# Performance work log

Measured on AMD Instinct MI355X. Metric: run time of the kernel, lower is better.

## Reference

```python
import jax, jax.numpy as jnp
import numpy as np

BN_EPS = 1e-5
W_SCALE = 0.05  # keep pre-softmax logits in a sane range with random weights


def setup_inputs() -> dict:
    key = jax.random.key(0)
    ks = jax.random.split(key, 8)
    b, C, H, W = 2, 512, 80, 80
    Ck, Cv, Co = 256, 256, 512
    return {
        "x": jax.random.normal(ks[0], (b, C, H, W), dtype=jnp.float32),
        "wk": jax.random.normal(ks[1], (Ck, C), dtype=jnp.float32) * W_SCALE,
        "bk": jax.random.normal(ks[2], (Ck,), dtype=jnp.float32) * W_SCALE,
        "gamma": jnp.ones((Ck,), dtype=jnp.float32),
        "beta": jnp.zeros((Ck,), dtype=jnp.float32),
        "rmean": jnp.zeros((Ck,), dtype=jnp.float32),
        "rvar": jnp.ones((Ck,), dtype=jnp.float32),
        "wv": jax.random.normal(ks[3], (Cv, C), dtype=jnp.float32) * W_SCALE,
        "bv": jax.random.normal(ks[4], (Cv,), dtype=jnp.float32) * W_SCALE,
        "wW": jax.random.normal(ks[5], (Co, Cv), dtype=jnp.float32) * W_SCALE,
        "bW": jax.random.normal(ks[6], (Co,), dtype=jnp.float32) * W_SCALE,
    }


def reference(x, wk, bk, gamma, beta, rmean, rvar, wv, bv, wW, bW):
    b, C, H, Wd = x.shape
    N = H * Wd
    Ck = wk.shape[0]
    Cv = wv.shape[0]
    # f_key == f_query (shared module): 1x1 conv + BN(inference) + ReLU
    k = jnp.einsum('bchw,oc->bohw', x, wk) + bk[:, None, None]
    scale_bn = gamma / jnp.sqrt(rvar + BN_EPS)
    k = (k - rmean[:, None, None]) * scale_bn[:, None, None] + beta[:, None, None]
    k = jax.nn.relu(k).reshape(b, Ck, N)          # [b, Ck, N]
    q = jnp.transpose(k, (0, 2, 1))               # [b, N, Ck] (query shares weights with key)
    # f_value: plain 1x1 conv
    v = (jnp.einsum('bchw,oc->bohw', x, wv) + bv[:, None, None]).reshape(b, Cv, N)
    sim = jnp.einsum('bnc,bcm->bnm', q, k) * (Ck ** -0.5)  # [b, N, N]
    sim = jax.nn.softmax(sim, axis=-1)
    ctx = jnp.einsum('bnm,bvm->bvn', sim, v).reshape(b, Cv, H, Wd)
    out = jnp.einsum('bvhw,ov->bohw', ctx, wW) + bW[:, None, None]
    return out
```

## Files before the change

kernel.cpp:

```cpp
#include <hip/hip_runtime.h>
#include <stdint.h>

typedef __attribute__((ext_vector_type(8))) short bf16x8;
typedef __attribute__((ext_vector_type(4))) float f32x4;

__device__ __forceinline__ ushort f2bf(float f) {
    union { float f; uint32_t i; } v; v.f = f;
    uint32_t r = v.i + 0x7fff + ((v.i >> 16) & 1);
    return (ushort)(r >> 16);
}
__device__ __forceinline__ uint32_t cvtpk(float lo, float hi) {
    uint32_t r;
    asm("v_cvt_pk_bf16_f32 %0, %1, %2" : "=v"(r) : "v"(lo), "v"(hi));
    return r;
}

typedef unsigned int uint_as1 __attribute__((address_space(1)));
typedef unsigned int uint_as3 __attribute__((address_space(3)));
__device__ __forceinline__ void async16(const void* g, void* l) {
    __builtin_amdgcn_global_load_lds((const uint_as1*)g, (uint_as3*)l, 16, 0, 0);
}


__global__ void cvt_f32_bf16(const float* __restrict__ in, ushort* __restrict__ out, int n) {
    int i = blockIdx.x * blockDim.x + threadIdx.x;
    if (i < n) out[i] = f2bf(in[i]);
}

__global__ void prep_bn(const float* __restrict__ bk, const float* __restrict__ gamma,
                        const float* __restrict__ beta, const float* __restrict__ rmean,
                        const float* __restrict__ rvar,
                        float* __restrict__ scaleA, float* __restrict__ shiftA) {
    int i = threadIdx.x;
    float s = gamma[i] * rsqrtf(rvar[i] + 1e-5f);
    scaleA[i] = 0.25f * s;
    shiftA[i] = 0.25f * ((bk[i] - rmean[i]) * s + beta[i]);
}

__global__ void transpose_cvt(const float* __restrict__ x, ushort* __restrict__ xt) {
    __shared__ float t[32][33];
    int b = blockIdx.z;
    int n0 = blockIdx.x * 32, c0 = blockIdx.y * 32;
    const float* xb = x + (size_t)b * 512 * 6400;
    ushort* xtb = xt + (size_t)b * 6400 * 512;
    int tx = threadIdx.x, ty = threadIdx.y;
    t[ty][tx] = xb[(size_t)(c0 + ty) * 6400 + n0 + tx];
    __syncthreads();
    xtb[(size_t)(n0 + ty) * 512 + c0 + tx] = f2bf(t[tx][ty]);
}

template <int EPI>
__global__ __launch_bounds__(256) void gemm_nt(
    const ushort* __restrict__ A, const ushort* __restrict__ B, void* __restrict__ Cout,
    int K, int lda, int ldb, int ldc,
    size_t zsa, size_t zsb, size_t zsc,
    const float* __restrict__ vec0, const float* __restrict__ vec1,
    float* __restrict__ rsum) {
    __shared__ __align__(16) ushort smem[6 * 4096];

    A += (size_t)blockIdx.z * zsa;
    B += (size_t)blockIdx.z * zsb;

    const int tid = threadIdx.x;
    const int lane = tid & 63, wave = tid >> 6;
    const int wm = wave & 1, wn = wave >> 1;
    const int bM = blockIdx.y * 128, bN = blockIdx.x * 128;

    const int sr = lane >> 2;
    const int scs = ((lane & 3) ^ ((lane >> 3) & 3)) * 8;
    const ushort* gA0 = A + (size_t)(bM + wave * 32 + sr) * lda + scs;
    const ushort* gA1 = gA0 + (size_t)16 * lda;
    const ushort* gB0 = B + (size_t)(bN + wave * 32 + sr) * ldb + scs;
    const ushort* gB1 = gB0 + (size_t)16 * ldb;
    ushort* lAw = &smem[wave * 1024];
    ushort* lBw = &smem[3 * 4096 + wave * 1024];

    const int rowA = wm * 64;
    const int rowB = wn * 64;
    const int fr = lane & 15;
    const int fk = ((lane >> 4) ^ ((fr >> 1) & 3)) * 8;

    f32x4 acc[4][4] = {};
    const int nT = K >> 5;

    auto stage = [&](int t, int buf) {
        const int k0 = t * 32;
        const int ob = buf * 4096;
        async16(gA0 + k0, lAw + ob);
        async16(gA1 + k0, lAw + ob + 512);
        async16(gB0 + k0, lBw + ob);
        async16(gB1 + k0, lBw + ob + 512);
    };

    stage(0, 0);
    if (nT > 1) stage(1, 1);

    for (int t = 0; t < nT; ++t) {
        if (t + 1 < nT) { asm volatile("s_waitcnt vmcnt(4)" ::: "memory"); }
        else            { asm volatile("s_waitcnt vmcnt(0)" ::: "memory"); }
        __builtin_amdgcn_sched_barrier(0);
        __builtin_amdgcn_s_barrier();
        __builtin_amdgcn_sched_barrier(0);
        if (t + 2 < nT) stage(t + 2, (t + 2) % 3);
        const int cur = t % 3;
        const ushort* lA = &smem[cur * 4096];
        const ushort* lB = &smem[3 * 4096 + cur * 4096];
        bf16x8 af[4], bff[4];
#pragma unroll
        for (int mi = 0; mi < 4; mi++)
            af[mi] = *(const bf16x8*)&lA[(rowA + mi * 16 + fr) * 32 + fk];
#pragma unroll
        for (int ni = 0; ni < 4; ni++)
            bff[ni] = *(const bf16x8*)&lB[(rowB + ni * 16 + fr) * 32 + fk];
#pragma unroll
        for (int mi = 0; mi < 4; mi++)
#pragma unroll
            for (int ni = 0; ni < 4; ni++)
                acc[mi][ni] = __builtin_amdgcn_mfma_f32_16x16x32_bf16(af[mi], bff[ni], acc[mi][ni], 0, 0, 0);
        __builtin_amdgcn_sched_barrier(0);
    }
    __builtin_amdgcn_s_barrier();
    __builtin_amdgcn_sched_barrier(0);

    float* Cf = (float*)Cout + (size_t)blockIdx.z * zsc;
    ushort* Cu = (ushort*)Cout + (size_t)blockIdx.z * zsc;
    float* lt = (float*)smem;
    const int g4 = (lane >> 4) * 4;
    const int cl = lane & 15;
    const int lr = tid >> 3;
    const int ch = tid & 7;

#pragma unroll
    for (int mi = 0; mi < 4; ++mi) {
#pragma unroll
        for (int ni = 0; ni < 4; ++ni) {
            const int lcol = wn * 64 + ni * 16 + cl;
#pragma unroll
            for (int r = 0; r < 4; ++r)
                lt[(wm * 16 + g4 + r) * 132 + lcol] = acc[mi][ni][r];
        }
        __syncthreads();
        {
            const int brow = (lr < 16) ? (mi * 16 + lr) : (64 + mi * 16 + (lr - 16));
            const int grow = bM + brow;
            const int gcol = bN + ch * 16;
            float vv[16];
#pragma unroll
            for (int i = 0; i < 16; i += 4) {
                f32x4 q = *(const f32x4*)&lt[lr * 132 + ch * 16 + i];
                vv[i] = q[0]; vv[i + 1] = q[1]; vv[i + 2] = q[2]; vv[i + 3] = q[3];
            }
            if (EPI == 1) {
#pragma unroll
                for (int i = 0; i < 16; i++)
                    vv[i] = fmaxf(vv[i] * vec0[gcol + i] + vec1[gcol + i], 0.f);
            }
            if (EPI == 2 || EPI == 3) {
                const float rb = vec0[grow];
#pragma unroll
                for (int i = 0; i < 16; i++) vv[i] += rb;
            }
            if (EPI == 5) {
                float ssum = 0.f;
#pragma unroll
                for (int i = 0; i < 16; i++) { vv[i] = __expf(vv[i]); ssum += vv[i]; }
                ssum += __shfl_down(ssum, 4, 8);
                ssum += __shfl_down(ssum, 2, 8);
                ssum += __shfl_down(ssum, 1, 8);
                if (ch == 0) rsum[(size_t)blockIdx.x * 6400 + grow] = ssum;
            }
            if (EPI == 3 || EPI == 4) {
#pragma unroll
                for (int i = 0; i < 16; i += 4) {
                    f32x4 q = { vv[i], vv[i + 1], vv[i + 2], vv[i + 3] };
                    *(f32x4*)&Cf[(size_t)grow * ldc + gcol + i] = q;
                }
            } else {
                uint4 q0 = { cvtpk(vv[0], vv[1]), cvtpk(vv[2], vv[3]),
                             cvtpk(vv[4], vv[5]), cvtpk(vv[6], vv[7]) };
                uint4 q1 = { cvtpk(vv[8], vv[9]), cvtpk(vv[10], vv[11]),
                             cvtpk(vv[12], vv[13]), cvtpk(vv[14], vv[15]) };
                *(uint4*)&Cu[(size_t)grow * ldc + gcol] = q0;
                *(uint4*)&Cu[(size_t)grow * ldc + gcol + 8] = q1;
            }
        }
        __syncthreads();
    }
}

__global__ __launch_bounds__(256) void combine_inv(const float* __restrict__ rsum,
                                                   float* __restrict__ inv) {
    int r = blockIdx.x * 256 + threadIdx.x;
    float s = 0.f;
#pragma unroll
    for (int xb = 0; xb < 50; xb++) s += rsum[(size_t)xb * 6400 + r];
    inv[r] = 1.f / s;
}

__global__ __launch_bounds__(256) void reduce_ctx(const float* __restrict__ part, ushort* __restrict__ ctx,
                                                  const float* __restrict__ inv) {
    const size_t CH = 1638400;
    size_t i = ((size_t)blockIdx.x * 256 + threadIdx.x) * 4;
    float4 a = *(const float4*)&part[i];
#pragma unroll
    for (int c = 1; c < 5; c++) {
        float4 s = *(const float4*)&part[i + (size_t)c * CH];
        a.x += s.x; a.y += s.y; a.z += s.z; a.w += s.w;
    }
    const float w = inv[i >> 8];
    uint2 o = { cvtpk(a.x * w, a.y * w), cvtpk(a.z * w, a.w * w) };
    *(uint2*)&ctx[i] = o;
}

extern "C" void kernel_launch(void* const* d_in, const int* in_sizes, int n_in,
                              void* d_out, int out_size, void* d_ws, size_t ws_size,
                              hipStream_t stream) {
    (void)in_sizes; (void)n_in; (void)out_size; (void)ws_size;
    const float* x     = (const float*)d_in[0];
    const float* wk    = (const float*)d_in[1];
    const float* bk    = (const float*)d_in[2];
    const float* gamma = (const float*)d_in[3];
    const float* beta  = (const float*)d_in[4];
    const float* rmean = (const float*)d_in[5];
    const float* rvar  = (const float*)d_in[6];
    const float* wv    = (const float*)d_in[7];
    const float* bv    = (const float*)d_in[8];
    const float* wW    = (const float*)d_in[9];
    const float* bW    = (const float*)d_in[10];
    float* out = (float*)d_out;

    ushort* Xt   = (ushort*)d_ws;
    ushort* wkb  = Xt + 6553600;
    ushort* wvb  = wkb + 131072;
    ushort* wWb  = wvb + 131072;
    ushort* Kt   = wWb + 131072;
    ushort* V    = Kt + 3276800;
    ushort* ctxT = V + 3276800;
    ushort* S    = ctxT + 3276800;
    float* scaleA = (float*)(S + 40960000);
    float* shiftA = scaleA + 256;
    float* rowsum = shiftA + 256;
    float* inv    = rowsum + 320000;
    float* part   = inv + 6400;

    cvt_f32_bf16<<<512, 256, 0, stream>>>(wk, wkb, 131072);
    cvt_f32_bf16<<<512, 256, 0, stream>>>(wv, wvb, 131072);
    cvt_f32_bf16<<<512, 256, 0, stream>>>(wW, wWb, 131072);
    prep_bn<<<1, 256, 0, stream>>>(bk, gamma, beta, rmean, rvar, scaleA, shiftA);
    transpose_cvt<<<dim3(200, 16, 2), dim3(32, 32), 0, stream>>>(x, Xt);

    gemm_nt<1><<<dim3(2, 50, 2), 256, 0, stream>>>(Xt, wkb, Kt, 512, 512, 512, 256,
                                                   3276800, 0, 1638400, scaleA, shiftA, nullptr);
    gemm_nt<2><<<dim3(50, 2, 2), 256, 0, stream>>>(wvb, Xt, V, 512, 512, 512, 6400,
                                                   0, 3276800, 1638400, bv, nullptr, nullptr);

    for (int b = 0; b < 2; b++) {
        ushort* Ktb  = Kt + (size_t)b * 1638400;
        ushort* Vb   = V  + (size_t)b * 1638400;
        ushort* ctxb = ctxT + (size_t)b * 1638400;
        gemm_nt<5><<<dim3(50, 50), 256, 0, stream>>>(Ktb, Ktb, S, 256, 256, 256, 6400,
                                                     0, 0, 0, nullptr, nullptr, rowsum);
        combine_inv<<<25, 256, 0, stream>>>(rowsum, inv);
        gemm_nt<4><<<dim3(2, 50, 5), 256, 0, stream>>>(S, Vb, part, 1280, 6400, 6400, 256,
                                                       1280, 1280, 1638400, nullptr, nullptr, nullptr);
        reduce_ctx<<<1600, 256, 0, stream>>>(part, ctxb, inv);
    }

    gemm_nt<3><<<dim3(50, 4, 2), 256, 0, stream>>>(wWb, ctxT, out, 256, 256, 256, 6400,
                                                   0, 1638400, 3276800, bW, nullptr, nullptr);
}
```

Before: 309.5 us.

## Add dedicated P·V GEMM kernel with register-held A operand and triple-buffered B

Replaces the generic gemm_nt<4> for the softmax-probabilities × V product with a specialized kernel. A fragments (S rows) are loaded straight from global memory into registers and prefetched two steps ahead, while only B (V) tiles go to LDS through async global_load_lds into a three-stage ring with one barrier per K step. The output is staged through LDS wave by wave for coalesced fp32 stores. The aim is to cut LDS traffic and barrier stalls in the largest GEMM, at the cost of more register pressure and uncoalesced direct global reads of A.

Result: slower. 319.7 us (+3.3%).

```diff
diff --git a/kernel.cpp b/kernel.cpp
--- a/kernel.cpp
+++ b/kernel.cpp
@@ -169,7 +169,7 @@
                 ssum += __shfl_down(ssum, 1, 8);
                 if (ch == 0) rsum[(size_t)blockIdx.x * 6400 + grow] = ssum;
             }
-            if (EPI == 3 || EPI == 4) {
+            if (EPI == 3) {
 #pragma unroll
                 for (int i = 0; i < 16; i += 4) {
                     f32x4 q = { vv[i], vv[i + 1], vv[i + 2], vv[i + 3] };
@@ -185,6 +185,106 @@
             }
         }
         __syncthreads();
+    }
+}
+
+__global__ __launch_bounds__(256) void gemm_pv(
+    const ushort* __restrict__ A, const ushort* __restrict__ B, float* __restrict__ Cout,
+    int K, int lda, int ldb, int ldc,
+    size_t zsa, size_t zsb, size_t zsc) {
+    __shared__ __align__(16) ushort smem[3 * 4096];
+
+    A += (size_t)blockIdx.z * zsa;
+    B += (size_t)blockIdx.z * zsb;
+
+    const int tid = threadIdx.x;
+    const int lane = tid & 63, wave = tid >> 6;
+    const int bM = blockIdx.y * 128, bN = blockIdx.x * 128;
+
+    const int sr = lane >> 2;
+    const int scs = ((lane & 3) ^ ((lane >> 3) & 3)) * 8;
+    const ushort* gB0 = B + (size_t)(bN + wave * 32 + sr) * ldb + scs;
+    const ushort* gB1 = gB0 + (size_t)16 * ldb;
+    ushort* lBw = &smem[wave * 1024];
+
+    const int fr = lane & 15;
+    const int fq = lane >> 4;
+    const int fk = (fq ^ ((fr >> 1) & 3)) * 8;
+
+    const ushort* gA0 = A + (size_t)(bM + wave * 32 + fr) * lda + fq * 8;
+    const ushort* gA1 = gA0 + (size_t)16 * lda;
+
+    f32x4 acc[2][8] = {};
+    const int nT = K >> 5;
+
+    auto stageB = [&](int t, int buf) {
+        const int k0 = t * 32;
+        const int ob = buf * 4096;
+        async16(gB0 + k0, lBw + ob);
+        async16(gB1 + k0, lBw + ob + 512);
+    };
+
+    stageB(0, 0);
+    bf16x8 a0E = *(const bf16x8*)&gA0[0];
+    bf16x8 a1E = *(const bf16x8*)&gA1[0];
+    stageB(1, 1);
+    bf16x8 a0O = *(const bf16x8*)&gA0[32];
+    bf16x8 a1O = *(const bf16x8*)&gA1[32];
+
+    auto body = [&](int t, bf16x8& a0S, bf16x8& a1S) {
+        if (t + 1 < nT) { asm volatile("s_waitcnt vmcnt(4)" ::: "memory"); }
+        else            { asm volatile("s_waitcnt vmcnt(0)" ::: "memory"); }
+        __builtin_amdgcn_sched_barrier(0);
+        __builtin_amdgcn_s_barrier();
+        __builtin_amdgcn_sched_barrier(0);
+        bf16x8 u0 = a0S, u1 = a1S;
+        if (t + 2 < nT) {
+            stageB(t + 2, (t + 2) % 3);
+            const int k0 = (t + 2) * 32;
+            a0S = *(const bf16x8*)&gA0[k0];
+            a1S = *(const bf16x8*)&gA1[k0];
+        }
+        const ushort* lB = &smem[(t % 3) * 4096];
+        bf16x8 bff[8];
+#pragma unroll
+        for (int ni = 0; ni < 8; ni++)
+            bff[ni] = *(const bf16x8*)&lB[(ni * 16 + fr) * 32 + fk];
+#pragma unroll
+        for (int ni = 0; ni < 8; ni++)
+            acc[0][ni] = __builtin_amdgcn_mfma_f32_16x16x32_bf16(u0, bff[ni], acc[0][ni], 0, 0, 0);
+#pragma unroll
+        for (int ni = 0; ni < 8; ni++)
+            acc[1][ni] = __builtin_amdgcn_mfma_f32_16x16x32_bf16(u1, bff[ni], acc[1][ni], 0, 0, 0);
+        __builtin_amdgcn_sched_barrier(0);
+    };
+
+    for (int i = 0; i < nT; i += 2) {
+        body(i, a0E, a1E);
+        body(i + 1, a0O, a1O);
+    }
+
+    float* Cf = Cout + (size_t)blockIdx.z * zsc;
+    float* lt = (float*)smem;
+    const int lr = tid >> 3;
+    const int ch = tid & 7;
+#pragma unroll
+    for (int ph = 0; ph < 4; ++ph) {
+        __syncthreads();
+        if (wave == ph) {
+#pragma unroll
+            for (int mi = 0; mi < 2; ++mi)
+#pragma unroll
+                for (int ni = 0; ni < 8; ++ni)
+#pragma unroll
+                    for (int r = 0; r < 4; ++r)
+                        lt[(mi * 16 + fq * 4 + r) * 132 + ni * 16 + fr] = acc[mi][ni][r];
+        }
+        __syncthreads();
+        const int grow = bM + ph * 32 + lr;
+        const int gcol = bN + ch * 16;
+#pragma unroll
+        for (int i = 0; i < 16; i += 4)
+            *(f32x4*)&Cf[(size_t)grow * ldc + gcol + i] = *(const f32x4*)&lt[lr * 132 + ch * 16 + i];
     }
 }
 
@@ -261,8 +361,8 @@
         gemm_nt<5><<<dim3(50, 50), 256, 0, stream>>>(Ktb, Ktb, S, 256, 256, 256, 6400,
                                                      0, 0, 0, nullptr, nullptr, rowsum);
         combine_inv<<<25, 256, 0, stream>>>(rowsum, inv);
-        gemm_nt<4><<<dim3(2, 50, 5), 256, 0, stream>>>(S, Vb, part, 1280, 6400, 6400, 256,
-                                                       1280, 1280, 1638400, nullptr, nullptr, nullptr);
+        gemm_pv<<<dim3(2, 50, 5), 256, 0, stream>>>(S, Vb, part, 1280, 6400, 6400, 256,
+                                                    1280, 1280, 1638400);
         reduce_ctx<<<1600, 256, 0, stream>>>(part, ctxb, inv);
     }
 
```

## Exploit symmetry of K^T K similarity to compute only upper-triangle tiles

Applied to the files above, without the earlier changes.

The similarity matrix is K^T K and therefore symmetric. The kernel now computes only the tiles with blockIdx.x >= blockIdx.y. Each off-diagonal tile writes its exp values both directly and transposed through shared memory into the mirrored tile, and computes the column partial row sums for the mirrored tile. This roughly halves the MFMA work for the largest GEMM. In exchange it adds an LDS transpose, extra barriers and half the blocks exit idle, so the grid is load-imbalanced.

After: 311.6 us. About the same (+0.7%).

```diff
diff --git a/kernel.cpp b/kernel.cpp
--- a/kernel.cpp
+++ b/kernel.cpp
@@ -56,6 +56,8 @@
     size_t zsa, size_t zsb, size_t zsc,
     const float* __restrict__ vec0, const float* __restrict__ vec1,
     float* __restrict__ rsum) {
+    if (EPI == 6 && blockIdx.x < blockIdx.y) return;
+
     __shared__ __align__(16) ushort smem[6 * 4096];
 
     A += (size_t)blockIdx.z * zsa;
@@ -130,6 +132,76 @@
     const int lr = tid >> 3;
     const int ch = tid & 7;
 
+    if (EPI == 6) {
+        const bool diag = (blockIdx.x == blockIdx.y);
+        float creg[16];
+#pragma unroll
+        for (int i = 0; i < 16; i++) creg[i] = 0.f;
+#pragma unroll
+        for (int mi = 0; mi < 4; ++mi) {
+#pragma unroll
+            for (int ni = 0; ni < 4; ++ni) {
+                const int lcol = wn * 64 + ni * 16 + cl;
+#pragma unroll
+                for (int r = 0; r < 4; ++r)
+                    lt[(wm * 16 + g4 + r) * 132 + lcol] = acc[mi][ni][r];
+            }
+            __syncthreads();
+            const int brow = (lr < 16) ? (mi * 16 + lr) : (64 + mi * 16 + (lr - 16));
+            const int grow = bM + brow;
+            const int gcol = bN + ch * 16;
+            float vv[16];
+#pragma unroll
+            for (int i = 0; i < 16; i += 4) {
+                f32x4 q = *(const f32x4*)&lt[lr * 132 + ch * 16 + i];
+                vv[i] = __expf(q[0]); vv[i + 1] = __expf(q[1]);
+                vv[i + 2] = __expf(q[2]); vv[i + 3] = __expf(q[3]);
+            }
+            float ssum = 0.f;
+#pragma unroll
+            for (int i = 0; i < 16; i++) { ssum += vv[i]; creg[i] += vv[i]; }
+            ssum += __shfl_down(ssum, 4, 8);
+            ssum += __shfl_down(ssum, 2, 8);
+            ssum += __shfl_down(ssum, 1, 8);
+            if (ch == 0) rsum[(size_t)blockIdx.x * 6400 + grow] = ssum;
+            uint4 q0 = { cvtpk(vv[0], vv[1]), cvtpk(vv[2], vv[3]),
+                         cvtpk(vv[4], vv[5]), cvtpk(vv[6], vv[7]) };
+            uint4 q1 = { cvtpk(vv[8], vv[9]), cvtpk(vv[10], vv[11]),
+                         cvtpk(vv[12], vv[13]), cvtpk(vv[14], vv[15]) };
+            *(uint4*)&Cu[(size_t)grow * ldc + gcol] = q0;
+            *(uint4*)&Cu[(size_t)grow * ldc + gcol + 8] = q1;
+            if (!diag) {
+#pragma unroll
+                for (int i = 0; i < 16; i++) lt[lr * 132 + ch * 16 + i] = vv[i];
+                __syncthreads();
+                const int j = tid >> 1, h = tid & 1;
+                ushort mo[16];
+#pragma unroll
+                for (int i = 0; i < 16; i += 2) {
+                    float a = lt[(h * 16 + i) * 132 + j];
+                    float b2 = lt[(h * 16 + i + 1) * 132 + j];
+                    *(uint32_t*)&mo[i] = cvtpk(a, b2);
+                }
+                const size_t mbase = (size_t)(bN + j) * ldc + bM + h * 64 + mi * 16;
+                *(uint4*)&Cu[mbase] = *(const uint4*)&mo[0];
+                *(uint4*)&Cu[mbase + 8] = *(const uint4*)&mo[8];
+            }
+            __syncthreads();
+        }
+        if (!diag) {
+#pragma unroll
+            for (int i = 0; i < 16; i++) lt[lr * 132 + ch * 16 + i] = creg[i];
+            __syncthreads();
+            if (tid < 128) {
+                float s = 0.f;
+#pragma unroll
+                for (int r = 0; r < 32; r++) s += lt[r * 132 + tid];
+                rsum[(size_t)blockIdx.y * 6400 + bN + tid] = s;
+            }
+        }
+        return;
+    }
+
 #pragma unroll
     for (int mi = 0; mi < 4; ++mi) {
 #pragma unroll
@@ -159,15 +231,6 @@
                 const float rb = vec0[grow];
 #pragma unroll
                 for (int i = 0; i < 16; i++) vv[i] += rb;
-            }
-            if (EPI == 5) {
-                float ssum = 0.f;
-#pragma unroll
-                for (int i = 0; i < 16; i++) { vv[i] = __expf(vv[i]); ssum += vv[i]; }
-                ssum += __shfl_down(ssum, 4, 8);
-                ssum += __shfl_down(ssum, 2, 8);
-                ssum += __shfl_down(ssum, 1, 8);
-                if (ch == 0) rsum[(size_t)blockIdx.x * 6400 + grow] = ssum;
             }
             if (EPI == 3 || EPI == 4) {
 #pragma unroll
@@ -258,7 +321,7 @@
         ushort* Ktb  = Kt + (size_t)b * 1638400;
         ushort* Vb   = V  + (size_t)b * 1638400;
         ushort* ctxb = ctxT + (size_t)b * 1638400;
-        gemm_nt<5><<<dim3(50, 50), 256, 0, stream>>>(Ktb, Ktb, S, 256, 256, 256, 6400,
+        gemm_nt<6><<<dim3(50, 50), 256, 0, stream>>>(Ktb, Ktb, S, 256, 256, 256, 6400,
                                                      0, 0, 0, nullptr, nullptr, rowsum);
         combine_inv<<<25, 256, 0, stream>>>(rowsum, inv);
         gemm_nt<4><<<dim3(2, 50, 5), 256, 0, stream>>>(S, Vb, part, 1280, 6400, 6400, 256,
```
